# Performance work log

Hardware: AMD Instinct MI355X
Metric: run time of the kernel (lower is better)

Reference implementation:

```python
import jax, jax.numpy as jnp
import numpy as np

EPS = 1e-05
GROUPS = 8


def setup_inputs() -> dict:
    key = jax.random.key(0)
    k1, k2, k3 = jax.random.split(key, 3)
    N, C, H, W = 32, 256, 56, 56
    x = jax.random.normal(k1, (N, C, H, W), dtype=jnp.float32)
    weight = jnp.ones((C,), dtype=jnp.float32)
    bias = jnp.zeros((C,), dtype=jnp.float32)
    gate_logits = jnp.array([2.8, 0.2, 1.1], dtype=jnp.float32)
    diag_proj = jnp.array([[0.08, -0.05, 0.08],
                           [-0.03, 0.08, -0.01],
                           [-0.05, -0.04, -0.07]], dtype=jnp.float32)
    return {"x": x, "weight": weight, "bias": bias,
            "gate_logits": gate_logits, "diag_proj": diag_proj}


def reference(x, weight, bias, gate_logits, diag_proj):
    xf = x.astype(jnp.float32)
    N, C, H, W = xf.shape

    # variance descriptor (differentiable: first-instance path recomputes without detach)
    batch_var = jnp.var(xf, axis=(0, 2, 3)).mean()    # per-channel var -> mean
    sample_var = jnp.var(xf, axis=(1, 2, 3)).mean()   # per-sample var -> mean
    channel_var = jnp.var(xf, axis=1).mean()          # var over channels at each (n,h,w) -> mean
    desc = jnp.tanh(jnp.log(jnp.maximum(jnp.stack([batch_var, sample_var, channel_var]), EPS)))

    gate = jax.nn.softmax(gate_logits + diag_proj @ desc)  # [3]

    # batch norm (training mode: batch statistics over N,H,W per channel)
    mu_b = xf.mean(axis=(0, 2, 3), keepdims=True)
    var_b = xf.var(axis=(0, 2, 3), keepdims=True)
    x_bn = (xf - mu_b) / jnp.sqrt(var_b + EPS)

    # layer norm = group_norm with 1 group: per-sample stats over C,H,W
    mu_l = xf.mean(axis=(1, 2, 3), keepdims=True)
    var_l = xf.var(axis=(1, 2, 3), keepdims=True)
    x_ln = (xf - mu_l) / jnp.sqrt(var_l + EPS)

    # group norm with GROUPS groups
    xg = xf.reshape(N, GROUPS, C // GROUPS, H, W)
    mu_g = xg.mean(axis=(2, 3, 4), keepdims=True)
    var_g = xg.var(axis=(2, 3, 4), keepdims=True)
    x_gn = ((xg - mu_g) / jnp.sqrt(var_g + EPS)).reshape(N, C, H, W)

    mixed = gate[0] * x_bn + gate[1] * x_ln + gate[2] * x_gn
    y = mixed * weight[None, :, None, None] + bias[None, :, None, None]
    return y.astype(x.dtype)
```

## Files before the change

### kernel.cpp

```cpp
#include <hip/hip_runtime.h>
#include <hip/hip_bf16.h>

#define NN 32
#define CC 256
#define HW 3136
#define HW4 784
#define CHW 802816
#define CHW4 200704
#define NCHW 25690112
#define GROUPS 8
#define CPG 32
#define NHW 100352
#define GHW 100352
#define EPSF 1e-5f

#define PB16 49
#define NSTAT (NN*PB16)
#define NPT2 NSTAT

typedef float f32x4 __attribute__((ext_vector_type(4)));

__global__ __launch_bounds__(256) void stats_kernel(
    const float4* __restrict__ x4,
    float* __restrict__ S1p, float* __restrict__ S2p,
    float* __restrict__ pT2)
{
    const int bx = blockIdx.x;
    const int n = bx / PB16, pb = bx - n * PB16;
    const int tid = threadIdx.x;
    const int w = tid >> 6, lane = tid & 63;
    const int cl = lane >> 3;
    const int pl = lane & 7;
    const int P0 = pb * 16;

    const float4* base = x4 + (size_t)n * CHW4 + P0 + pl;

    float s1a[8], s2a[8];
    float4 T0 = make_float4(0.f, 0.f, 0.f, 0.f);
    float4 T1 = make_float4(0.f, 0.f, 0.f, 0.f);
    #pragma unroll
    for (int k = 0; k < 8; ++k) {
        const int c = (k * 4 + w) * 8 + cl;
        float4 v0 = base[(size_t)c * HW4];
        float4 v1 = base[(size_t)c * HW4 + 8];
        T0.x += v0.x; T0.y += v0.y; T0.z += v0.z; T0.w += v0.w;
        T1.x += v1.x; T1.y += v1.y; T1.z += v1.z; T1.w += v1.w;
        s1a[k] = v0.x + v0.y + v0.z + v0.w + v1.x + v1.y + v1.z + v1.w;
        s2a[k] = v0.x*v0.x + v0.y*v0.y + v0.z*v0.z + v0.w*v0.w
               + v1.x*v1.x + v1.y*v1.y + v1.z*v1.z + v1.w*v1.w;
    }

    #pragma unroll
    for (int k = 0; k < 8; ++k) {
        #pragma unroll
        for (int off = 1; off < 8; off <<= 1) {
            s1a[k] += __shfl_down(s1a[k], off, 64);
            s2a[k] += __shfl_down(s2a[k], off, 64);
        }
    }
    if (pl == 0) {
        #pragma unroll
        for (int k = 0; k < 8; ++k) {
            const int c = (k * 4 + w) * 8 + cl;
            S1p[(size_t)bx * 256 + c] = s1a[k];
            S2p[(size_t)bx * 256 + c] = s2a[k];
        }
    }

    #pragma unroll
    for (int off = 8; off < 64; off <<= 1) {
        T0.x += __shfl_xor(T0.x, off, 64);
        T0.y += __shfl_xor(T0.y, off, 64);
        T0.z += __shfl_xor(T0.z, off, 64);
        T0.w += __shfl_xor(T0.w, off, 64);
        T1.x += __shfl_xor(T1.x, off, 64);
        T1.y += __shfl_xor(T1.y, off, 64);
        T1.z += __shfl_xor(T1.z, off, 64);
        T1.w += __shfl_xor(T1.w, off, 64);
    }
    __shared__ float4 shT[4][16];
    if (lane < 8) {
        shT[w][pl] = T0;
        shT[w][8 + pl] = T1;
    }
    __syncthreads();
    if (tid < 16) {
        float4 a = shT[0][tid], b = shT[1][tid], c4 = shT[2][tid], d = shT[3][tid];
        const float tx = a.x + b.x + c4.x + d.x;
        const float ty = a.y + b.y + c4.y + d.y;
        const float tz = a.z + b.z + c4.z + d.z;
        const float tw = a.w + b.w + c4.w + d.w;
        float t2 = tx*tx + ty*ty + tz*tz + tw*tw;
        #pragma unroll
        for (int off = 1; off < 16; off <<= 1) t2 += __shfl_down(t2, off, 64);
        if (tid == 0) pT2[bx] = t2;
    }
}

__global__ __launch_bounds__(256) void fold_kernel(
    const float* __restrict__ S1p, const float* __restrict__ S2p,
    float* __restrict__ S1, float* __restrict__ S2)
{
    const int n = blockIdx.x, c = threadIdx.x;
    const float* p1 = S1p + (size_t)n * PB16 * 256 + c;
    const float* p2 = S2p + (size_t)n * PB16 * 256 + c;
    float a = 0.f, b = 0.f;
    #pragma unroll 7
    for (int pb = 0; pb < PB16; ++pb) {
        a += p1[(size_t)pb * 256];
        b += p2[(size_t)pb * 256];
    }
    S1[n * 256 + c] = a;
    S2[n * 256 + c] = b;
}

__global__ __launch_bounds__(256) void finalize_kernel(
    const float* __restrict__ S1, const float* __restrict__ S2,
    const float* __restrict__ partialT2,
    const float* __restrict__ weight, const float* __restrict__ bias,
    const float* __restrict__ gate_logits, const float* __restrict__ diag_proj,
    float* __restrict__ A, float* __restrict__ B)
{
    const int tid = threadIdx.x;
    __shared__ float sh_mu_b[CC], sh_rs_b[CC];
    __shared__ float sh_mu_g[NN * GROUPS], sh_rs_g[NN * GROUPS];
    __shared__ float sh_mu_l[NN], sh_rs_l[NN];
    __shared__ float sh_red1[4], sh_red2[4], sh_red3[4], sh_red4[4];
    __shared__ float sh_gate[3];

    const float inv_NHW  = 1.f / (float)NHW;
    const float inv_CHW  = 1.f / (float)CHW;
    const float inv_GHW  = 1.f / (float)GHW;
    const float inv_NCHW = 1.f / (float)NCHW;

    const int c = tid;
    float s1 = 0.f, s2 = 0.f;
    for (int n = 0; n < NN; ++n) { s1 += S1[n * CC + c]; s2 += S2[n * CC + c]; }
    const float mu_b  = s1 * inv_NHW;
    const float var_b = s2 * inv_NHW - mu_b * mu_b;
    sh_mu_b[c] = mu_b;
    sh_rs_b[c] = rsqrtf(var_b + EPSF);

    const int ng_n = tid >> 3, ng_g = tid & 7;
    float s1g = 0.f, s2g = 0.f;
    for (int cc2 = 0; cc2 < CPG; ++cc2) {
        const int idx = ng_n * CC + ng_g * CPG + cc2;
        s1g += S1[idx]; s2g += S2[idx];
    }
    const float mu_g  = s1g * inv_GHW;
    const float var_g = s2g * inv_GHW - mu_g * mu_g;
    sh_mu_g[tid] = mu_g;
    sh_rs_g[tid] = rsqrtf(var_g + EPSF);

    float s1l = s1g, s2l = s2g;
    #pragma unroll
    for (int off = 1; off < 8; off <<= 1) {
        s1l += __shfl_xor(s1l, off, 64);
        s2l += __shfl_xor(s2l, off, 64);
    }
    float var_l_contrib = 0.f;
    if (ng_g == 0) {
        const float mu_l  = s1l * inv_CHW;
        const float var_l = s2l * inv_CHW - mu_l * mu_l;
        sh_mu_l[ng_n] = mu_l;
        sh_rs_l[ng_n] = rsqrtf(var_l + EPSF);
        var_l_contrib = var_l;
    }

    float t2p = 0.f;
    for (int i = tid; i < NPT2; i += 256) t2p += partialT2[i];

    float r1 = var_b, r2 = s2, r3 = var_l_contrib, r4 = t2p;
    #pragma unroll
    for (int off = 32; off; off >>= 1) {
        r1 += __shfl_down(r1, off, 64);
        r2 += __shfl_down(r2, off, 64);
        r3 += __shfl_down(r3, off, 64);
        r4 += __shfl_down(r4, off, 64);
    }
    const int wave = tid >> 6, lane = tid & 63;
    if (lane == 0) { sh_red1[wave] = r1; sh_red2[wave] = r2; sh_red3[wave] = r3; sh_red4[wave] = r4; }
    __syncthreads();
    if (tid == 0) {
        const float sum_var_b = sh_red1[0] + sh_red1[1] + sh_red1[2] + sh_red1[3];
        const float total_x2  = sh_red2[0] + sh_red2[1] + sh_red2[2] + sh_red2[3];
        const float sum_var_l = sh_red3[0] + sh_red3[1] + sh_red3[2] + sh_red3[3];
        const float sum_T2    = sh_red4[0] + sh_red4[1] + sh_red4[2] + sh_red4[3];

        const float batch_var   = sum_var_b * (1.f / (float)CC);
        const float sample_var  = sum_var_l * (1.f / (float)NN);
        const float channel_var = total_x2 * inv_NCHW
                                - sum_T2 * inv_NHW * (1.f / ((float)CC * (float)CC));

        float desc[3];
        desc[0] = tanhf(logf(fmaxf(batch_var,   EPSF)));
        desc[1] = tanhf(logf(fmaxf(sample_var,  EPSF)));
        desc[2] = tanhf(logf(fmaxf(channel_var, EPSF)));

        float lg[3];
        #pragma unroll
        for (int i = 0; i < 3; ++i) {
            lg[i] = gate_logits[i] + diag_proj[i*3+0]*desc[0]
                                   + diag_proj[i*3+1]*desc[1]
                                   + diag_proj[i*3+2]*desc[2];
        }
        const float m = fmaxf(lg[0], fmaxf(lg[1], lg[2]));
        const float e0 = expf(lg[0]-m), e1 = expf(lg[1]-m), e2 = expf(lg[2]-m);
        const float inv = 1.f / (e0 + e1 + e2);
        sh_gate[0] = e0 * inv; sh_gate[1] = e1 * inv; sh_gate[2] = e2 * inv;
    }
    __syncthreads();

    const float g0 = sh_gate[0], g1 = sh_gate[1], g2 = sh_gate[2];
    for (int i = tid; i < NN * CC; i += 256) {
        const int n = i >> 8, ch = i & 255, g = ch >> 5;
        const float w = weight[ch], bi = bias[ch];
        const float rb = sh_rs_b[ch], rl = sh_rs_l[n], rg = sh_rs_g[n*8+g];
        const float mb = sh_mu_b[ch], ml = sh_mu_l[n], mg = sh_mu_g[n*8+g];
        const float scale = g0*rb + g1*rl + g2*rg;
        const float offs  = g0*mb*rb + g1*ml*rl + g2*mg*rg;
        A[i] = w * scale;
        B[i] = bi - w * offs;
    }
}

__global__ __launch_bounds__(256) void apply_kernel(
    const f32x4* __restrict__ x4, const float* __restrict__ A,
    const float* __restrict__ B, f32x4* __restrict__ y4)
{
    const int nc = blockIdx.x;
    const float a = A[nc], b = B[nc];
    const f32x4* xp = x4 + (size_t)nc * HW4;
    f32x4* yp = y4 + (size_t)nc * HW4;
    for (int i = threadIdx.x; i < HW4; i += 256) {
        f32x4 v = xp[i];
        f32x4 r;
        r.x = fmaf(v.x, a, b);
        r.y = fmaf(v.y, a, b);
        r.z = fmaf(v.z, a, b);
        r.w = fmaf(v.w, a, b);
        __builtin_nontemporal_store(r, &yp[i]);
    }
}

extern "C" void kernel_launch(void* const* d_in, const int* in_sizes, int n_in,
                              void* d_out, int out_size, void* d_ws, size_t ws_size,
                              hipStream_t stream) {
    const float* x           = (const float*)d_in[0];
    const float* weight      = (const float*)d_in[1];
    const float* bias        = (const float*)d_in[2];
    const float* gate_logits = (const float*)d_in[3];
    const float* diag_proj   = (const float*)d_in[4];
    float* out = (float*)d_out;

    float* ws   = (float*)d_ws;
    float* S1p  = ws;
    float* S2p  = ws + 401408;
    float* S1   = ws + 802816;
    float* S2   = ws + 811008;
    float* A    = ws + 819200;
    float* B    = ws + 827392;
    float* pT2  = ws + 835584;

    stats_kernel<<<NSTAT, 256, 0, stream>>>((const float4*)x, S1p, S2p, pT2);
    fold_kernel<<<NN, 256, 0, stream>>>(S1p, S2p, S1, S2);
    finalize_kernel<<<1, 256, 0, stream>>>(S1, S2, pT2, weight, bias,
                                           gate_logits, diag_proj, A, B);
    apply_kernel<<<NN * CC, 256, 0, stream>>>((const f32x4*)x, A, B, (f32x4*)out);
}
```

Before: 66.13 us.

## Interleave partial stats, move per-(n,c) coefficient computation into apply kernel

Partial sums S1/S2 are stored interleaved as float2, so the fold and finalize kernels each issue one load per element instead of two. The single-block finalize kernel no longer runs the 8192-iteration loop that built the A/B coefficient arrays. It only writes compact per-channel, per-sample and per-group mean/rstd plus the gate. Each apply block recomputes its scale and offset from these small tables, and the apply loop is fully unrolled into three or four vector loads issued up front. This shortens the serial single-block stage in exchange for a few redundant scalar loads per apply block.

```diff
diff --git a/kernel.cpp b/kernel.cpp
--- a/kernel.cpp
+++ b/kernel.cpp
@@ -22,7 +22,7 @@
 
 __global__ __launch_bounds__(256) void stats_kernel(
     const float4* __restrict__ x4,
-    float* __restrict__ S1p, float* __restrict__ S2p,
+    float2* __restrict__ S12p,
     float* __restrict__ pT2)
 {
     const int bx = blockIdx.x;
@@ -62,8 +62,7 @@
         #pragma unroll
         for (int k = 0; k < 8; ++k) {
             const int c = (k * 4 + w) * 8 + cl;
-            S1p[(size_t)bx * 256 + c] = s1a[k];
-            S2p[(size_t)bx * 256 + c] = s2a[k];
+            S12p[(size_t)bx * 256 + c] = make_float2(s1a[k], s2a[k]);
         }
     }
 
@@ -98,35 +97,27 @@
 }
 
 __global__ __launch_bounds__(256) void fold_kernel(
-    const float* __restrict__ S1p, const float* __restrict__ S2p,
-    float* __restrict__ S1, float* __restrict__ S2)
+    const float2* __restrict__ S12p, float2* __restrict__ S12)
 {
     const int n = blockIdx.x, c = threadIdx.x;
-    const float* p1 = S1p + (size_t)n * PB16 * 256 + c;
-    const float* p2 = S2p + (size_t)n * PB16 * 256 + c;
+    const float2* p = S12p + (size_t)n * PB16 * 256 + c;
     float a = 0.f, b = 0.f;
     #pragma unroll 7
     for (int pb = 0; pb < PB16; ++pb) {
-        a += p1[(size_t)pb * 256];
-        b += p2[(size_t)pb * 256];
-    }
-    S1[n * 256 + c] = a;
-    S2[n * 256 + c] = b;
+        float2 v = p[(size_t)pb * 256];
+        a += v.x; b += v.y;
+    }
+    S12[n * 256 + c] = make_float2(a, b);
 }
 
 __global__ __launch_bounds__(256) void finalize_kernel(
-    const float* __restrict__ S1, const float* __restrict__ S2,
-    const float* __restrict__ partialT2,
-    const float* __restrict__ weight, const float* __restrict__ bias,
+    const float2* __restrict__ S12, const float* __restrict__ partialT2,
     const float* __restrict__ gate_logits, const float* __restrict__ diag_proj,
-    float* __restrict__ A, float* __restrict__ B)
+    float2* __restrict__ CB, float2* __restrict__ CL, float2* __restrict__ CG,
+    float* __restrict__ GT)
 {
     const int tid = threadIdx.x;
-    __shared__ float sh_mu_b[CC], sh_rs_b[CC];
-    __shared__ float sh_mu_g[NN * GROUPS], sh_rs_g[NN * GROUPS];
-    __shared__ float sh_mu_l[NN], sh_rs_l[NN];
     __shared__ float sh_red1[4], sh_red2[4], sh_red3[4], sh_red4[4];
-    __shared__ float sh_gate[3];
 
     const float inv_NHW  = 1.f / (float)NHW;
     const float inv_CHW  = 1.f / (float)CHW;
@@ -135,22 +126,23 @@
 
     const int c = tid;
     float s1 = 0.f, s2 = 0.f;
-    for (int n = 0; n < NN; ++n) { s1 += S1[n * CC + c]; s2 += S2[n * CC + c]; }
+    for (int n = 0; n < NN; ++n) {
+        float2 v = S12[n * CC + c];
+        s1 += v.x; s2 += v.y;
+    }
     const float mu_b  = s1 * inv_NHW;
     const float var_b = s2 * inv_NHW - mu_b * mu_b;
-    sh_mu_b[c] = mu_b;
-    sh_rs_b[c] = rsqrtf(var_b + EPSF);
+    CB[c] = make_float2(mu_b, rsqrtf(var_b + EPSF));
 
     const int ng_n = tid >> 3, ng_g = tid & 7;
     float s1g = 0.f, s2g = 0.f;
     for (int cc2 = 0; cc2 < CPG; ++cc2) {
-        const int idx = ng_n * CC + ng_g * CPG + cc2;
-        s1g += S1[idx]; s2g += S2[idx];
+        float2 v = S12[ng_n * CC + ng_g * CPG + cc2];
+        s1g += v.x; s2g += v.y;
     }
     const float mu_g  = s1g * inv_GHW;
     const float var_g = s2g * inv_GHW - mu_g * mu_g;
-    sh_mu_g[tid] = mu_g;
-    sh_rs_g[tid] = rsqrtf(var_g + EPSF);
+    CG[tid] = make_float2(mu_g, rsqrtf(var_g + EPSF));
 
     float s1l = s1g, s2l = s2g;
     #pragma unroll
@@ -162,8 +154,7 @@
     if (ng_g == 0) {
         const float mu_l  = s1l * inv_CHW;
         const float var_l = s2l * inv_CHW - mu_l * mu_l;
-        sh_mu_l[ng_n] = mu_l;
-        sh_rs_l[ng_n] = rsqrtf(var_l + EPSF);
+        CL[ng_n] = make_float2(mu_l, rsqrtf(var_l + EPSF));
         var_l_contrib = var_l;
     }
 
@@ -207,39 +198,47 @@
         const float m = fmaxf(lg[0], fmaxf(lg[1], lg[2]));
         const float e0 = expf(lg[0]-m), e1 = expf(lg[1]-m), e2 = expf(lg[2]-m);
         const float inv = 1.f / (e0 + e1 + e2);
-        sh_gate[0] = e0 * inv; sh_gate[1] = e1 * inv; sh_gate[2] = e2 * inv;
-    }
-    __syncthreads();
-
-    const float g0 = sh_gate[0], g1 = sh_gate[1], g2 = sh_gate[2];
-    for (int i = tid; i < NN * CC; i += 256) {
-        const int n = i >> 8, ch = i & 255, g = ch >> 5;
-        const float w = weight[ch], bi = bias[ch];
-        const float rb = sh_rs_b[ch], rl = sh_rs_l[n], rg = sh_rs_g[n*8+g];
-        const float mb = sh_mu_b[ch], ml = sh_mu_l[n], mg = sh_mu_g[n*8+g];
-        const float scale = g0*rb + g1*rl + g2*rg;
-        const float offs  = g0*mb*rb + g1*ml*rl + g2*mg*rg;
-        A[i] = w * scale;
-        B[i] = bi - w * offs;
+        GT[0] = e0 * inv; GT[1] = e1 * inv; GT[2] = e2 * inv;
     }
 }
 
 __global__ __launch_bounds__(256) void apply_kernel(
-    const f32x4* __restrict__ x4, const float* __restrict__ A,
-    const float* __restrict__ B, f32x4* __restrict__ y4)
+    const f32x4* __restrict__ x4,
+    const float* __restrict__ weight, const float* __restrict__ bias,
+    const float2* __restrict__ CB, const float2* __restrict__ CL,
+    const float2* __restrict__ CG, const float* __restrict__ GT,
+    f32x4* __restrict__ y4)
 {
     const int nc = blockIdx.x;
-    const float a = A[nc], b = B[nc];
+    const int n = nc >> 8, ch = nc & 255, g = ch >> 5;
+    const float g0 = GT[0], g1 = GT[1], g2 = GT[2];
+    const float2 cb = CB[ch], cl2 = CL[n], cg2 = CG[n * 8 + g];
+    const float w = weight[ch], bi = bias[ch];
+    const float scale = g0 * cb.y + g1 * cl2.y + g2 * cg2.y;
+    const float offs  = g0 * cb.x * cb.y + g1 * cl2.x * cl2.y + g2 * cg2.x * cg2.y;
+    const float a = w * scale;
+    const float b = fmaf(-w, offs, bi);
+
     const f32x4* xp = x4 + (size_t)nc * HW4;
     f32x4* yp = y4 + (size_t)nc * HW4;
-    for (int i = threadIdx.x; i < HW4; i += 256) {
-        f32x4 v = xp[i];
-        f32x4 r;
-        r.x = fmaf(v.x, a, b);
-        r.y = fmaf(v.y, a, b);
-        r.z = fmaf(v.z, a, b);
-        r.w = fmaf(v.w, a, b);
-        __builtin_nontemporal_store(r, &yp[i]);
+    const int tid = threadIdx.x;
+
+    f32x4 v0 = xp[tid];
+    f32x4 v1 = xp[tid + 256];
+    f32x4 v2 = xp[tid + 512];
+    f32x4 v3;
+    if (tid < 16) v3 = xp[tid + 768];
+
+    f32x4 r0, r1, r2, r3;
+    r0.x = fmaf(v0.x, a, b); r0.y = fmaf(v0.y, a, b); r0.z = fmaf(v0.z, a, b); r0.w = fmaf(v0.w, a, b);
+    r1.x = fmaf(v1.x, a, b); r1.y = fmaf(v1.y, a, b); r1.z = fmaf(v1.z, a, b); r1.w = fmaf(v1.w, a, b);
+    r2.x = fmaf(v2.x, a, b); r2.y = fmaf(v2.y, a, b); r2.z = fmaf(v2.z, a, b); r2.w = fmaf(v2.w, a, b);
+    __builtin_nontemporal_store(r0, &yp[tid]);
+    __builtin_nontemporal_store(r1, &yp[tid + 256]);
+    __builtin_nontemporal_store(r2, &yp[tid + 512]);
+    if (tid < 16) {
+        r3.x = fmaf(v3.x, a, b); r3.y = fmaf(v3.y, a, b); r3.z = fmaf(v3.z, a, b); r3.w = fmaf(v3.w, a, b);
+        __builtin_nontemporal_store(r3, &yp[tid + 768]);
     }
 }
 
@@ -254,17 +253,18 @@
     float* out = (float*)d_out;
 
     float* ws   = (float*)d_ws;
-    float* S1p  = ws;
-    float* S2p  = ws + 401408;
-    float* S1   = ws + 802816;
-    float* S2   = ws + 811008;
-    float* A    = ws + 819200;
-    float* B    = ws + 827392;
-    float* pT2  = ws + 835584;
-
-    stats_kernel<<<NSTAT, 256, 0, stream>>>((const float4*)x, S1p, S2p, pT2);
-    fold_kernel<<<NN, 256, 0, stream>>>(S1p, S2p, S1, S2);
-    finalize_kernel<<<1, 256, 0, stream>>>(S1, S2, pT2, weight, bias,
-                                           gate_logits, diag_proj, A, B);
-    apply_kernel<<<NN * CC, 256, 0, stream>>>((const f32x4*)x, A, B, (f32x4*)out);
-}
+    float2* S12p = (float2*)ws;
+    float2* S12  = (float2*)(ws + 802816);
+    float2* CB   = (float2*)(ws + 819200);
+    float2* CL   = (float2*)(ws + 819712);
+    float2* CG   = (float2*)(ws + 819776);
+    float*  GT   = ws + 820288;
+    float*  pT2  = ws + 820296;
+
+    stats_kernel<<<NSTAT, 256, 0, stream>>>((const float4*)x, S12p, pT2);
+    fold_kernel<<<NN, 256, 0, stream>>>(S12p, S12);
+    finalize_kernel<<<1, 256, 0, stream>>>(S12, pT2, gate_logits, diag_proj,
+                                           CB, CL, CG, GT);
+    apply_kernel<<<NN * CC, 256, 0, stream>>>((const f32x4*)x, weight, bias,
+                                              CB, CL, CG, GT, (f32x4*)out);
+}
```

New measurement: 62.82 us. 5.0% less time.
